# Kernel optimization log

Measured on AMD Instinct MI355X. Metric: run time of the kernel, lower is better.

The kernel has to match this reference:

```python
import jax, jax.numpy as jnp
from jax import lax
import numpy as np

B, C, H, W = 16, 64, 256, 256
K = 7


def setup_inputs() -> dict:
    key = jax.random.key(0)
    kx, kk = jax.random.split(key)
    x = jax.random.normal(kx, (B, C, H, W), dtype=jnp.float32)
    kernel = jax.random.normal(kk, (K, K), dtype=jnp.float32)
    return {"x": x, "kernel": kernel}


def reference(x, kernel):
    # Depthwise conv: every (b, ch) slice convolved with the SAME [K,K] kernel.
    # scipy-style true convolution => flip the kernel, 'same' padding.
    c = x.shape[1]
    kflip = jnp.flip(kernel, axis=(0, 1))
    w = jnp.tile(kflip[None, None], (c, 1, 1, 1))  # [C,1,K,K]
    y = lax.conv_general_dilated(
        x, w,
        window_strides=(1, 1),
        padding='SAME',
        feature_group_count=c,
        dimension_numbers=('NCHW', 'OIHW', 'NCHW'),
    )
    # mish(y) = y * tanh(softplus(y))
    return y * jnp.tanh(jax.nn.softplus(y))
```

## Files before the change

### kernel.cpp

```cpp
#include <hip/hip_runtime.h>


#define HW 256
#define PITCH 80
#define LROWS 70
#define NSTG 1400
#define TPB 8

typedef _Float16 f16x8 __attribute__((ext_vector_type(8)));
typedef float    f32x4 __attribute__((ext_vector_type(4)));
typedef __fp16   h2    __attribute__((ext_vector_type(2)));
union U32H2 { unsigned u; h2 h; };
union BFU   { uint4 u; f16x8 h; };

__device__ __forceinline__ float mish_f(float y) {
    float t = __expf(y);
    float u = 1.0f + t;
    float d = __fmaf_rn(u, u, 1.0f);
    return y * (1.0f - __fdividef(2.0f, d));
}

__global__ __launch_bounds__(256)
__attribute__((amdgpu_waves_per_eu(4, 7)))
void dwconv7_mish_mfma6(const float* __restrict__ x,
                        const float* __restrict__ kern,
                        float* __restrict__ out) {
    __shared__ __align__(16) _Float16 lds_in[2][LROWS * PITCH];

    const int tid = threadIdx.x;
    const int bid = blockIdx.x;
    const int plane = bid >> 1;
    const int sbase = (bid & 1) << 3;

    const float* __restrict__ xp = x + (size_t)plane * (HW * HW);
    float* __restrict__ op = out + (size_t)plane * (HW * HW);

    unsigned* lds_B = (unsigned*)lds_in[1];

    float kf[49];
    #pragma unroll
    for (int i = 0; i < 49; ++i) {
        int p = i / 7, q = i - p * 7;
        kf[i] = __int_as_float(__builtin_amdgcn_readfirstlane(
                    __float_as_int(kern[(6 - p) * 7 + (6 - q)])));
    }

    {
        const int j  = tid >> 4;
        const int kw = tid & 15;
        #pragma unroll
        for (int p = 0; p < 7; ++p) {
            const int d0 = 2 * kw - j - 5;
            const int d1 = d0 + 1;
            float v0 = 0.f, v1 = 0.f;
            #pragma unroll
            for (int q = 0; q < 7; ++q) {
                v0 = (d0 == q) ? kf[p * 7 + q] : v0;
                v1 = (d1 == q) ? kf[p * 7 + q] : v1;
            }
            U32H2 u; u.h = __builtin_amdgcn_cvt_pkrtz(v0, v1);
            lds_B[p * 256 + tid] = u.u;
        }
    }

    int ro_[6], co_[6];
    #pragma unroll
    for (int it = 0; it < 6; ++it) {
        int idx = tid + it * 256;
        int r = idx / 20, g = idx - 20 * r;
        ro_[it] = r - 3;
        co_[it] = 4 * g - 8;
    }

    {
        const int c0 = (sbase & 3) << 6, r0 = (sbase >> 2) << 6;
        #pragma unroll
        for (int it = 0; it < 6; ++it) {
            if (it < 5 || tid < NSTG - 1280) {
                int gr = r0 + ro_[it], gc = c0 + co_[it];
                float4 f = make_float4(0.f, 0.f, 0.f, 0.f);
                if ((unsigned)gr < (unsigned)HW && (unsigned)gc <= (unsigned)(HW - 4))
                    f = *(const float4*)(xp + (gr << 8) + gc);
                U32H2 a, b;
                a.h = __builtin_amdgcn_cvt_pkrtz(f.x, f.y);
                b.h = __builtin_amdgcn_cvt_pkrtz(f.z, f.w);
                ((uint2*)lds_in[0])[tid + it * 256] = make_uint2(a.u, b.u);
            }
        }
    }
    __syncthreads();

    const int lane = tid & 63;
    const int w    = tid >> 6;
    const int lrow = lane & 15;
    const int lk   = lane >> 4;

    f16x8 bfrag[7];
    #pragma unroll
    for (int p = 0; p < 7; ++p) {
        BFU bu;
        bu.u = ((const uint4*)lds_B)[p * 64 + lrow * 4 + lk];
        bfrag[p] = bu.h;
    }
    __syncthreads();

    float4 rf[6];

    #pragma unroll 1
    for (int t = 0; t < TPB; ++t) {
        const int s  = sbase + t;
        const int c0 = (s & 3) << 6, r0 = (s >> 2) << 6;

        if (t + 1 < TPB) {
            const int s2 = sbase + t + 1;
            const int c2 = (s2 & 3) << 6, r2 = (s2 >> 2) << 6;
            #pragma unroll
            for (int it = 0; it < 6; ++it) {
                if (it < 5 || tid < NSTG - 1280) {
                    int gr = r2 + ro_[it], gc = c2 + co_[it];
                    rf[it] = make_float4(0.f, 0.f, 0.f, 0.f);
                    if ((unsigned)gr < (unsigned)HW && (unsigned)gc <= (unsigned)(HW - 4))
                        rf[it] = *(const float4*)(xp + (gr << 8) + gc);
                }
            }
        }
        __builtin_amdgcn_sched_barrier(0);

        const _Float16* bufp = lds_in[t & 1];
        #pragma unroll
        for (int t4 = 0; t4 < 4; ++t4) {
            f32x4 acc = {0.f, 0.f, 0.f, 0.f};
            #pragma unroll
            for (int p = 0; p < 7; ++p) {
                f16x8 a = *(const f16x8*)(bufp +
                            (16 * w + lrow + p) * PITCH + 16 * t4 + 8 * lk);
                acc = __builtin_amdgcn_mfma_f32_16x16x32_f16(a, bfrag[p], acc,
                                                             0, 0, 0);
            }
            const int col   = c0 + 16 * t4 + lrow;
            const int rbase = r0 + 16 * w + 4 * lk;
            op[(rbase + 0) * HW + col] = mish_f(acc[0]);
            op[(rbase + 1) * HW + col] = mish_f(acc[1]);
            op[(rbase + 2) * HW + col] = mish_f(acc[2]);
            op[(rbase + 3) * HW + col] = mish_f(acc[3]);
        }
        __builtin_amdgcn_sched_barrier(0);

        if (t + 1 < TPB) {
            #pragma unroll
            for (int it = 0; it < 6; ++it) {
                if (it < 5 || tid < NSTG - 1280) {
                    U32H2 a, b;
                    a.h = __builtin_amdgcn_cvt_pkrtz(rf[it].x, rf[it].y);
                    b.h = __builtin_amdgcn_cvt_pkrtz(rf[it].z, rf[it].w);
                    ((uint2*)lds_in[(t + 1) & 1])[tid + it * 256] = make_uint2(a.u, b.u);
                }
            }
        }

        asm volatile("s_waitcnt lgkmcnt(0)\n\ts_barrier" ::: "memory");
        __builtin_amdgcn_sched_barrier(0);
    }
}

extern "C" void kernel_launch(void* const* d_in, const int* in_sizes, int n_in,
                              void* d_out, int out_size, void* d_ws, size_t ws_size,
                              hipStream_t stream) {
    const float* x = (const float*)d_in[0];
    const float* k = (const float*)d_in[1];
    float* out = (float*)d_out;

    dim3 grid(2 * 16 * 64, 1, 1);
    dim3 block(256);
    dwconv7_mish_mfma6<<<grid, block, 0, stream>>>(x, k, out);
}
```

Baseline: 128.1 us.

## Replace per-tile halo loads with full-width rolling row ring buffer

Each block now owns a 128-row strip of one plane at full 256-column width and streams 16 new input rows per step into a 40-row LDS ring. The earlier scheme double-buffered independently haloed 64x64 tiles. This removes redundant halo reloads across tiles and shrinks LDS use from two tile buffers to one ring, which allows higher occupancy (waves_per_eu raised). It adds modular ring indexing, and prefetched rows overwrite slots in the same ring instead of a separate buffer.

Result: slower. 266.0 us (+107.6%).

```diff
diff --git a/kernel.cpp b/kernel.cpp
--- a/kernel.cpp
+++ b/kernel.cpp
@@ -2,9 +2,8 @@
 
 
 #define HW 256
-#define PITCH 80
-#define LROWS 70
-#define NSTG 1400
+#define RING 40
+#define PITCH 272
 #define TPB 8
 
 typedef _Float16 f16x8 __attribute__((ext_vector_type(8)));
@@ -21,21 +20,26 @@
 }
 
 __global__ __launch_bounds__(256)
-__attribute__((amdgpu_waves_per_eu(4, 7)))
-void dwconv7_mish_mfma6(const float* __restrict__ x,
-                        const float* __restrict__ kern,
-                        float* __restrict__ out) {
-    __shared__ __align__(16) _Float16 lds_in[2][LROWS * PITCH];
+__attribute__((amdgpu_waves_per_eu(6, 8)))
+void dwconv7_mish_ring(const float* __restrict__ x,
+                       const float* __restrict__ kern,
+                       float* __restrict__ out) {
+    __shared__ __align__(16) _Float16 ring[RING * PITCH];
+    unsigned* lds_B = (unsigned*)ring;
 
-    const int tid = threadIdx.x;
-    const int bid = blockIdx.x;
+    const int tid  = threadIdx.x;
+    const int lane = tid & 63;
+    const int w    = tid >> 6;
+    const int lrow = lane & 15;
+    const int lk   = lane >> 4;
+    const int c0   = w << 6;
+
+    const int bid   = blockIdx.x;
     const int plane = bid >> 1;
-    const int sbase = (bid & 1) << 3;
+    const int r0    = (bid & 1) << 7;
 
     const float* __restrict__ xp = x + (size_t)plane * (HW * HW);
     float* __restrict__ op = out + (size_t)plane * (HW * HW);
-
-    unsigned* lds_B = (unsigned*)lds_in[1];
 
     float kf[49];
     #pragma unroll
@@ -62,99 +66,91 @@
             lds_B[p * 256 + tid] = u.u;
         }
     }
-
-    int ro_[6], co_[6];
-    #pragma unroll
-    for (int it = 0; it < 6; ++it) {
-        int idx = tid + it * 256;
-        int r = idx / 20, g = idx - 20 * r;
-        ro_[it] = r - 3;
-        co_[it] = 4 * g - 8;
-    }
-
-    {
-        const int c0 = (sbase & 3) << 6, r0 = (sbase >> 2) << 6;
-        #pragma unroll
-        for (int it = 0; it < 6; ++it) {
-            if (it < 5 || tid < NSTG - 1280) {
-                int gr = r0 + ro_[it], gc = c0 + co_[it];
-                float4 f = make_float4(0.f, 0.f, 0.f, 0.f);
-                if ((unsigned)gr < (unsigned)HW && (unsigned)gc <= (unsigned)(HW - 4))
-                    f = *(const float4*)(xp + (gr << 8) + gc);
-                U32H2 a, b;
-                a.h = __builtin_amdgcn_cvt_pkrtz(f.x, f.y);
-                b.h = __builtin_amdgcn_cvt_pkrtz(f.z, f.w);
-                ((uint2*)lds_in[0])[tid + it * 256] = make_uint2(a.u, b.u);
-            }
-        }
-    }
     __syncthreads();
-
-    const int lane = tid & 63;
-    const int w    = tid >> 6;
-    const int lrow = lane & 15;
-    const int lk   = lane >> 4;
 
     f16x8 bfrag[7];
     #pragma unroll
     for (int p = 0; p < 7; ++p) {
         BFU bu;
-        bu.u = ((const uint4*)lds_B)[p * 64 + lrow * 4 + lk];
+        bu.u = ((const uint4*)lds_B)[(p << 6) + (lrow << 2) + lk];
         bfrag[p] = bu.h;
     }
     __syncthreads();
 
-    float4 rf[6];
+    if (tid < 160) {
+        int row = tid >> 2, q = tid & 3;
+        ((uint2*)ring)[row * 68 + (q < 2 ? q : 64 + q)] = make_uint2(0u, 0u);
+    }
+
+    #pragma unroll
+    for (int i = 0; i < 6; ++i) {
+        const int row = w + 4 * i;
+        if (row < 22) {
+            const int gr = r0 - 3 + row;
+            const int slot = (gr + RING) % RING;
+            float4 f = make_float4(0.f, 0.f, 0.f, 0.f);
+            if ((unsigned)gr < (unsigned)HW)
+                f = *(const float4*)(xp + (gr << 8) + 4 * lane);
+            U32H2 a, b;
+            a.h = __builtin_amdgcn_cvt_pkrtz(f.x, f.y);
+            b.h = __builtin_amdgcn_cvt_pkrtz(f.z, f.w);
+            ((uint2*)ring)[slot * 68 + 2 + lane] = make_uint2(a.u, b.u);
+        }
+    }
+    __syncthreads();
+
+    float4 rf[4];
 
     #pragma unroll 1
     for (int t = 0; t < TPB; ++t) {
-        const int s  = sbase + t;
-        const int c0 = (s & 3) << 6, r0 = (s >> 2) << 6;
+        const int W = r0 + (t << 4);
 
         if (t + 1 < TPB) {
-            const int s2 = sbase + t + 1;
-            const int c2 = (s2 & 3) << 6, r2 = (s2 >> 2) << 6;
             #pragma unroll
-            for (int it = 0; it < 6; ++it) {
-                if (it < 5 || tid < NSTG - 1280) {
-                    int gr = r2 + ro_[it], gc = c2 + co_[it];
-                    rf[it] = make_float4(0.f, 0.f, 0.f, 0.f);
-                    if ((unsigned)gr < (unsigned)HW && (unsigned)gc <= (unsigned)(HW - 4))
-                        rf[it] = *(const float4*)(xp + (gr << 8) + gc);
-                }
+            for (int i = 0; i < 4; ++i) {
+                const int gr = W + 19 + w + 4 * i;
+                rf[i] = make_float4(0.f, 0.f, 0.f, 0.f);
+                if (gr < HW)
+                    rf[i] = *(const float4*)(xp + (gr << 8) + 4 * lane);
             }
         }
         __builtin_amdgcn_sched_barrier(0);
 
-        const _Float16* bufp = lds_in[t & 1];
+        const int b0 = (W + 37) % RING;
+        int sa[7];
+        #pragma unroll
+        for (int p = 0; p < 7; ++p) {
+            int s = b0 + lrow + p;
+            s -= (s >= RING) ? RING : 0;
+            sa[p] = s * PITCH;
+        }
         #pragma unroll
         for (int t4 = 0; t4 < 4; ++t4) {
             f32x4 acc = {0.f, 0.f, 0.f, 0.f};
             #pragma unroll
             for (int p = 0; p < 7; ++p) {
-                f16x8 a = *(const f16x8*)(bufp +
-                            (16 * w + lrow + p) * PITCH + 16 * t4 + 8 * lk);
+                f16x8 a = *(const f16x8*)(ring + sa[p] + c0 + 16 * t4 + 8 * lk);
                 acc = __builtin_amdgcn_mfma_f32_16x16x32_f16(a, bfrag[p], acc,
                                                              0, 0, 0);
             }
-            const int col   = c0 + 16 * t4 + lrow;
-            const int rbase = r0 + 16 * w + 4 * lk;
-            op[(rbase + 0) * HW + col] = mish_f(acc[0]);
-            op[(rbase + 1) * HW + col] = mish_f(acc[1]);
-            op[(rbase + 2) * HW + col] = mish_f(acc[2]);
-            op[(rbase + 3) * HW + col] = mish_f(acc[3]);
+            const int col = c0 + 16 * t4 + lrow;
+            const int rb  = W + (lk << 2);
+            op[(rb + 0) * HW + col] = mish_f(acc[0]);
+            op[(rb + 1) * HW + col] = mish_f(acc[1]);
+            op[(rb + 2) * HW + col] = mish_f(acc[2]);
+            op[(rb + 3) * HW + col] = mish_f(acc[3]);
         }
         __builtin_amdgcn_sched_barrier(0);
 
         if (t + 1 < TPB) {
             #pragma unroll
-            for (int it = 0; it < 6; ++it) {
-                if (it < 5 || tid < NSTG - 1280) {
-                    U32H2 a, b;
-                    a.h = __builtin_amdgcn_cvt_pkrtz(rf[it].x, rf[it].y);
-                    b.h = __builtin_amdgcn_cvt_pkrtz(rf[it].z, rf[it].w);
-                    ((uint2*)lds_in[(t + 1) & 1])[tid + it * 256] = make_uint2(a.u, b.u);
-                }
+            for (int i = 0; i < 4; ++i) {
+                const int gr = W + 19 + w + 4 * i;
+                const int slot = gr % RING;
+                U32H2 a, b;
+                a.h = __builtin_amdgcn_cvt_pkrtz(rf[i].x, rf[i].y);
+                b.h = __builtin_amdgcn_cvt_pkrtz(rf[i].z, rf[i].w);
+                ((uint2*)ring)[slot * 68 + 2 + lane] = make_uint2(a.u, b.u);
             }
         }
 
@@ -172,5 +168,5 @@
 
     dim3 grid(2 * 16 * 64, 1, 1);
     dim3 block(256);
-    dwconv7_mish_mfma6<<<grid, block, 0, stream>>>(x, k, out);
+    dwconv7_mish_ring<<<grid, block, 0, stream>>>(x, k, out);
 }
```
